# Kernel optimization log

Measured on AMD Instinct MI355X. Metric: run time of the kernel, lower is better.

Reference implementation:

```python
import jax, jax.numpy as jnp
import numpy as np

B, H, W = 8, 1024, 1024
RADIUS = 15.0
THRESHOLD_VOTES = 0.01
THRESHOLD_PEAKS = 0.2
KSIZE_VOTES = 15
KSIZE_PEAKS = 17


def setup_inputs() -> dict:
    key = jax.random.key(0)
    k1, k2 = jax.random.split(key)
    return {
        "stem_keypoint_output": jax.random.uniform(k1, (B, 1, H, W), dtype=jnp.float32),
        "stem_offset_output": jax.random.normal(k2, (B, 2, H, W), dtype=jnp.float32),
    }


def reference(stem_keypoint_output, stem_offset_output):
    b = stem_keypoint_output.shape[0]
    xs = jnp.arange(W, dtype=jnp.float32)[None, :]   # (1, W)
    ys = jnp.arange(H, dtype=jnp.float32)[:, None]   # (H, 1)

    # vote target coordinates, (B, H, W)
    votes_xs = jnp.round(xs + RADIUS * stem_offset_output[:, 0]).astype(jnp.int32)
    votes_ys = jnp.round(ys + RADIUS * stem_offset_output[:, 1]).astype(jnp.int32)
    weights = stem_keypoint_output[:, 0]

    # zero out-of-bounds and low-confidence votes (matches the index-assignment zeroing)
    valid = (votes_xs >= 0) & (votes_xs < W) & (votes_ys >= 0) & (votes_ys < H) & (weights >= THRESHOLD_VOTES)
    weights = jnp.where(valid, weights, 0.0)
    votes_xs = jnp.clip(votes_xs, 0, W - 1)
    votes_ys = jnp.clip(votes_ys, 0, H - 1)

    # scatter-accumulate votes (flat global index = b*H*W + y*W + x)
    flat_idx = (jnp.arange(b, dtype=jnp.int32)[:, None, None] * (H * W)
                + votes_ys * W + votes_xs).ravel()
    votes = jnp.zeros(b * H * W, jnp.float32).at[flat_idx].add(weights.ravel()).reshape(b, H, W)
    votes = votes / (np.pi * RADIUS * RADIUS)

    # box filter (conv with all-ones kernel, zero bias, SAME padding) == windowed sum
    votes = jax.lax.reduce_window(votes, 0.0, jax.lax.add,
                                  (1, KSIZE_VOTES, KSIZE_VOTES), (1, 1, 1), 'SAME')
    # max-pool dilation, SAME padding
    votes_dilated = jax.lax.reduce_window(votes, -jnp.inf, jax.lax.max,
                                          (1, KSIZE_PEAKS, KSIZE_PEAKS), (1, 1, 1), 'SAME')

    peaks = jnp.isclose(votes, votes_dilated) & (votes > THRESHOLD_PEAKS)
    # Return fixed-shape outputs: accumulated vote map (B,1,H,W) and peak mask (B,H,W).
    # (The original extracts (x, y, score) triplets per slice via nonzero(), which is
    #  data-dependent; the mask + vote map carry the identical information.)
    return votes[:, None], peaks
```

## Files before the change

### kernel.cpp

```cpp
#include <hip/hip_runtime.h>

constexpr int BB = 8;
constexpr int HH = 1024;
constexpr int WW = 1024;
constexpr int HW = HH * WW;
constexpr int TOTAL = BB * HW;

constexpr float RADIUS = 15.0f;
constexpr float THR_VOTES = 0.01f;
constexpr float THR_PEAKS = 0.2f;
constexpr float DIVISOR = 706.8583470577035f;

constexpr int TS = 64;
constexpr int AP = 48;
constexpr int RG = TS + 2 * AP;
constexpr int RGF = RG / 4;
constexpr int NF4 = RG * RGF;
constexpr int TPB = 256;
constexpr int NBLK = 2048;
constexpr int FCAP = 128;

constexpr int FIDX0 = NBLK;
constexpr int FW0   = NBLK + NBLK * FCAP;

__device__ __forceinline__ void process4(int px0, int py, float4 kw, float4 fox,
                                         float4 foy, int tx0, int ty0, int b,
                                         float* tile, int* lcnt,
                                         int* lidx, float* lw) {
    const float w[4]  = {kw.x, kw.y, kw.z, kw.w};
    const float ox[4] = {fox.x, fox.y, fox.z, fox.w};
    const float oy[4] = {foy.x, foy.y, foy.z, foy.w};
#pragma unroll
    for (int j = 0; j < 4; ++j) {
        const int px = px0 + j;
        const float fx = __fadd_rn((float)px, __fmul_rn(RADIUS, ox[j]));
        const float fy = __fadd_rn((float)py, __fmul_rn(RADIUS, oy[j]));
        const int vx = (int)rintf(fx);
        const int vy = (int)rintf(fy);
        if (vx < 0 || vx >= WW || vy < 0 || vy >= HH || w[j] < THR_VOTES) continue;
        const int dx = vx - px, dy = vy - py;
        if (dx >= -AP && dx <= AP && dy >= -AP && dy <= AP) {
            const int lx = vx - tx0, ly = vy - ty0;
            if (lx >= 0 && lx < TS && ly >= 0 && ly < TS)
                atomicAdd(&tile[ly * TS + lx], w[j]);
        } else if (px >= tx0 && px < tx0 + TS && py >= ty0 && py < ty0 + TS) {
            const int slot = atomicAdd(lcnt, 1);
            if (slot < FCAP) {
                lidx[slot] = b * HW + vy * WW + vx;
                lw[slot]   = w[j];
            }
        }
    }
}

__global__ __launch_bounds__(TPB, 8)
void gather_votes(const float* __restrict__ kp, const float* __restrict__ off,
                  float* __restrict__ vraw, float* __restrict__ farbuf) {
    __shared__ float tile[TS * TS];
    __shared__ int   lidx[FCAP];
    __shared__ float lw[FCAP];
    __shared__ int   lcnt;
    const int blk = blockIdx.x;
    const int b   = blk & 7;
    const int t   = blk >> 3;
    const int ty0 = (t >> 4) * TS;
    const int tx0 = (t & 15) * TS;

    if (threadIdx.x == 0) lcnt = 0;
    float4* tf4 = (float4*)tile;
    for (int j = threadIdx.x; j < TS * TS / 4; j += TPB)
        tf4[j] = make_float4(0.f, 0.f, 0.f, 0.f);
    __syncthreads();

    const float* kpb  = kp  + (long)b * HW;
    const float* offx = off + (long)b * 2 * HW;
    const float* offy = offx + HW;

    for (int u = threadIdx.x; u < NF4; u += 2 * TPB) {
        const int uB = u + TPB;
        const int rA  = u / RGF;
        const int cA  = u - rA * RGF;
        const int pyA = ty0 - AP + rA;
        const int pxA = tx0 - AP + 4 * cA;
        const bool okA = (pyA >= 0 && pyA < HH && pxA >= 0 && pxA <= WW - 4);
        const int rB  = uB / RGF;
        const int cB  = uB - rB * RGF;
        const int pyB = ty0 - AP + rB;
        const int pxB = tx0 - AP + 4 * cB;
        const bool okB = (uB < NF4 && pyB >= 0 && pyB < HH && pxB >= 0 && pxB <= WW - 4);

        float4 kA, xA, yA, kB, xB, yB;
        if (okA) {
            const long p = (long)pyA * WW + pxA;
            kA = *(const float4*)(kpb + p);
            xA = *(const float4*)(offx + p);
            yA = *(const float4*)(offy + p);
        }
        if (okB) {
            const long p = (long)pyB * WW + pxB;
            kB = *(const float4*)(kpb + p);
            xB = *(const float4*)(offx + p);
            yB = *(const float4*)(offy + p);
        }
        if (okA) process4(pxA, pyA, kA, xA, yA, tx0, ty0, b, tile, &lcnt, lidx, lw);
        if (okB) process4(pxB, pyB, kB, xB, yB, tx0, ty0, b, tile, &lcnt, lidx, lw);
    }
    __syncthreads();

    float* vb = vraw + (long)b * HW;
    for (int j = threadIdx.x; j < TS * TS / 4; j += TPB) {
        const int r  = j / (TS / 4);
        const int c4 = j % (TS / 4);
        *(float4*)&vb[(ty0 + r) * WW + tx0 + c4 * 4] = tf4[j];
    }
    const int n = min(lcnt, FCAP);
    int* fi = (int*)farbuf;
    if (threadIdx.x == 0) fi[blk] = n;
    for (int j = threadIdx.x; j < n; j += TPB) {
        fi[FIDX0 + blk * FCAP + j] = lidx[j];
        farbuf[FW0 + blk * FCAP + j] = lw[j];
    }
}

__global__ void far_scatter(const float* __restrict__ farbuf,
                            float* __restrict__ vraw) {
    const int s = blockIdx.x * blockDim.x + threadIdx.x;
    if (s >= NBLK * FCAP) return;
    const int blk = s / FCAP;
    const int j   = s % FCAP;
    const int* fi = (const int*)farbuf;
    if (j < min(fi[blk], FCAP))
        atomicAdd(&vraw[fi[FIDX0 + blk * FCAP + j]], farbuf[FW0 + blk * FCAP + j]);
}

__global__ __launch_bounds__(256)
void box_row(const float* __restrict__ in, float* __restrict__ out) {
    const long base = (long)blockIdx.x * WW;
    const int c0 = threadIdx.x * 4;
    float v[20];
#pragma unroll
    for (int k = 0; k < 5; ++k) {
        const int c = c0 - 8 + 4 * k;
        float4 f = (c >= 0 && c <= WW - 4) ? *(const float4*)&in[base + c]
                                           : make_float4(0.f, 0.f, 0.f, 0.f);
        v[4 * k + 0] = f.x; v[4 * k + 1] = f.y;
        v[4 * k + 2] = f.z; v[4 * k + 3] = f.w;
    }
    float s = 0.f;
#pragma unroll
    for (int k = 1; k <= 15; ++k) s += v[k];
    float4 o;
    o.x = s / DIVISOR;
    s += v[16] - v[1];  o.y = s / DIVISOR;
    s += v[17] - v[2];  o.z = s / DIVISOR;
    s += v[18] - v[3];  o.w = s / DIVISOR;
    *(float4*)&out[base + c0] = o;
}

__global__ __launch_bounds__(256)
void box_col(const float* __restrict__ in, float* __restrict__ out) {
    const int bi = blockIdx.x;
    const int xg = bi & 3;
    const int rg = (bi >> 2) & 127;
    const int b  = bi >> 9;
    const int x  = xg * 256 + threadIdx.x;
    const int r0 = rg * 8;
    const float* p = in + (long)b * HW + x;
    float v[22];
#pragma unroll
    for (int k = 0; k < 22; ++k) {
        const int r = r0 - 7 + k;
        v[k] = (r >= 0 && r < HH) ? p[(long)r * WW] : 0.f;
    }
    float s = 0.f;
#pragma unroll
    for (int k = 0; k < 15; ++k) s += v[k];
    float* q = out + (long)b * HW + x;
    q[(long)r0 * WW] = s;
#pragma unroll
    for (int j = 1; j < 8; ++j) {
        s += v[14 + j] - v[j - 1];
        q[(long)(r0 + j) * WW] = s;
    }
}

__global__ __launch_bounds__(256)
void max_row(const float* __restrict__ in, float* __restrict__ out) {
    const long base = (long)blockIdx.x * WW;
    const int c0 = threadIdx.x * 4;
    float v[20];
#pragma unroll
    for (int k = 0; k < 5; ++k) {
        const int c = c0 - 8 + 4 * k;
        float4 f = (c >= 0 && c <= WW - 4)
                       ? *(const float4*)&in[base + c]
                       : make_float4(-INFINITY, -INFINITY, -INFINITY, -INFINITY);
        v[4 * k + 0] = f.x; v[4 * k + 1] = f.y;
        v[4 * k + 2] = f.z; v[4 * k + 3] = f.w;
    }
    float m = v[3];
#pragma unroll
    for (int k = 4; k <= 16; ++k) m = fmaxf(m, v[k]);
    float4 o;
    o.x = fmaxf(fmaxf(m, v[0]),  fmaxf(v[1],  v[2]));
    o.y = fmaxf(fmaxf(m, v[1]),  fmaxf(v[2],  v[17]));
    o.z = fmaxf(fmaxf(m, v[2]),  fmaxf(v[17], v[18]));
    o.w = fmaxf(fmaxf(m, v[17]), fmaxf(v[18], v[19]));
    *(float4*)&out[base + c0] = o;
}

__global__ __launch_bounds__(256)
void max_col_peaks(const float* __restrict__ rowmaxed,
                   const float* __restrict__ votes,
                   float* __restrict__ peaks) {
    const int bi = blockIdx.x;
    const int xg = bi & 3;
    const int rg = (bi >> 2) & 127;
    const int b  = bi >> 9;
    const int x  = xg * 256 + threadIdx.x;
    const int r0 = rg * 8;
    const float* p = rowmaxed + (long)b * HW + x;
    float v[24];
#pragma unroll
    for (int k = 0; k < 24; ++k) {
        const int r = r0 - 8 + k;
        v[k] = (r >= 0 && r < HH) ? p[(long)r * WW] : -INFINITY;
    }
    float suf[17];
    suf[16] = v[16];
#pragma unroll
    for (int k = 15; k >= 0; --k) suf[k] = fmaxf(v[k], suf[k + 1]);

    const float* vp = votes + (long)b * HW + x;
    float* q = peaks + (long)b * HW + x;
    float pre = -INFINITY;
#pragma unroll
    for (int j = 0; j < 8; ++j) {
        if (j > 0) pre = fmaxf(pre, v[16 + j]);
        const float d = fmaxf(suf[j], pre);
        const float vv = vp[(long)(r0 + j) * WW];
        const bool close = fabsf(vv - d) <= (1e-8f + 1e-5f * fabsf(d));
        q[(long)(r0 + j) * WW] = (close && vv > THR_PEAKS) ? 1.0f : 0.0f;
    }
}

extern "C" void kernel_launch(void* const* d_in, const int* in_sizes, int n_in,
                              void* d_out, int out_size, void* d_ws, size_t ws_size,
                              hipStream_t stream) {
    const float* kp  = (const float*)d_in[0];
    const float* off = (const float*)d_in[1];
    float* V = (float*)d_out;
    float* P = (float*)d_out + TOTAL;
    float* W = (float*)d_ws;

    gather_votes <<<NBLK, TPB, 0, stream>>>(kp, off, W, P);
    far_scatter  <<<NBLK * FCAP / 256, 256, 0, stream>>>(P, W);
    box_row      <<<8192, 256, 0, stream>>>(W, P);
    box_col      <<<4096, 256, 0, stream>>>(P, V);
    max_row      <<<8192, 256, 0, stream>>>(V, W);
    max_col_peaks<<<4096, 256, 0, stream>>>(W, V, P);
}
```

Before: 233.0 us.

## Fuse separable box and max filters into 2D shared-memory tiled kernels

```diff
diff --git a/kernel.cpp b/kernel.cpp
--- a/kernel.cpp
+++ b/kernel.cpp
@@ -22,6 +22,10 @@
 
 constexpr int FIDX0 = NBLK;
 constexpr int FW0   = NBLK + NBLK * FCAP;
+
+constexpr int BT = 64;
+constexpr int BH = 8;
+constexpr int BR = BT + 2 * BH;
 
 __device__ __forceinline__ void process4(int px0, int py, float4 kw, float4 fox,
                                          float4 foy, int tx0, int ty0, int b,
@@ -134,113 +138,125 @@
 }
 
 __global__ __launch_bounds__(256)
-void box_row(const float* __restrict__ in, float* __restrict__ out) {
-    const long base = (long)blockIdx.x * WW;
-    const int c0 = threadIdx.x * 4;
-    float v[20];
-#pragma unroll
-    for (int k = 0; k < 5; ++k) {
-        const int c = c0 - 8 + 4 * k;
-        float4 f = (c >= 0 && c <= WW - 4) ? *(const float4*)&in[base + c]
-                                           : make_float4(0.f, 0.f, 0.f, 0.f);
-        v[4 * k + 0] = f.x; v[4 * k + 1] = f.y;
-        v[4 * k + 2] = f.z; v[4 * k + 3] = f.w;
-    }
-    float s = 0.f;
-#pragma unroll
-    for (int k = 1; k <= 15; ++k) s += v[k];
-    float4 o;
-    o.x = s / DIVISOR;
-    s += v[16] - v[1];  o.y = s / DIVISOR;
-    s += v[17] - v[2];  o.z = s / DIVISOR;
-    s += v[18] - v[3];  o.w = s / DIVISOR;
-    *(float4*)&out[base + c0] = o;
+void box2d(const float* __restrict__ in, float* __restrict__ out) {
+    __shared__ float reg[BR * BR];
+    __shared__ float rs[BR * BT];
+    const int blk = blockIdx.x;
+    const int b   = blk & 7;
+    const int t   = blk >> 3;
+    const int ty0 = (t >> 4) * BT;
+    const int tx0 = (t & 15) * BT;
+    const float* ib = in + (long)b * HW;
+
+    for (int o = threadIdx.x; o < BR * (BR / 4); o += 256) {
+        const int r  = o / (BR / 4);
+        const int c4 = o % (BR / 4);
+        const int gy = ty0 - BH + r;
+        const int gx = tx0 - BH + 4 * c4;
+        float4 f = make_float4(0.f, 0.f, 0.f, 0.f);
+        if (gy >= 0 && gy < HH && gx >= 0 && gx <= WW - 4)
+            f = *(const float4*)&ib[(long)gy * WW + gx];
+        *(float4*)&reg[r * BR + 4 * c4] = f;
+    }
+    __syncthreads();
+
+    for (int o = threadIdx.x; o < BR * (BT / 4); o += 256) {
+        const int r = o >> 4;
+        const int c = (o & 15) * 4;
+        float v[20];
+#pragma unroll
+        for (int k = 0; k < 5; ++k) {
+            float4 f = *(const float4*)&reg[r * BR + c + 4 * k];
+            v[4 * k] = f.x; v[4 * k + 1] = f.y; v[4 * k + 2] = f.z; v[4 * k + 3] = f.w;
+        }
+        float s = 0.f;
+#pragma unroll
+        for (int k = 1; k <= 15; ++k) s += v[k];
+        float4 q;
+        q.x = s / DIVISOR;
+        s += v[16] - v[1];  q.y = s / DIVISOR;
+        s += v[17] - v[2];  q.z = s / DIVISOR;
+        s += v[18] - v[3];  q.w = s / DIVISOR;
+        *(float4*)&rs[r * BT + c] = q;
+    }
+    __syncthreads();
+
+    float* ob = out + (long)b * HW;
+    for (int o = threadIdx.x; o < BT * (BT / 4); o += 256) {
+        const int r = o >> 4;
+        const int c = (o & 15) * 4;
+        float4 s = make_float4(0.f, 0.f, 0.f, 0.f);
+#pragma unroll
+        for (int k = 1; k <= 15; ++k) {
+            float4 f = *(const float4*)&rs[(r + k) * BT + c];
+            s.x += f.x; s.y += f.y; s.z += f.z; s.w += f.w;
+        }
+        *(float4*)&ob[(long)(ty0 + r) * WW + tx0 + c] = s;
+    }
 }
 
 __global__ __launch_bounds__(256)
-void box_col(const float* __restrict__ in, float* __restrict__ out) {
-    const int bi = blockIdx.x;
-    const int xg = bi & 3;
-    const int rg = (bi >> 2) & 127;
-    const int b  = bi >> 9;
-    const int x  = xg * 256 + threadIdx.x;
-    const int r0 = rg * 8;
-    const float* p = in + (long)b * HW + x;
-    float v[22];
-#pragma unroll
-    for (int k = 0; k < 22; ++k) {
-        const int r = r0 - 7 + k;
-        v[k] = (r >= 0 && r < HH) ? p[(long)r * WW] : 0.f;
-    }
-    float s = 0.f;
-#pragma unroll
-    for (int k = 0; k < 15; ++k) s += v[k];
-    float* q = out + (long)b * HW + x;
-    q[(long)r0 * WW] = s;
-#pragma unroll
-    for (int j = 1; j < 8; ++j) {
-        s += v[14 + j] - v[j - 1];
-        q[(long)(r0 + j) * WW] = s;
-    }
-}
-
-__global__ __launch_bounds__(256)
-void max_row(const float* __restrict__ in, float* __restrict__ out) {
-    const long base = (long)blockIdx.x * WW;
-    const int c0 = threadIdx.x * 4;
-    float v[20];
-#pragma unroll
-    for (int k = 0; k < 5; ++k) {
-        const int c = c0 - 8 + 4 * k;
-        float4 f = (c >= 0 && c <= WW - 4)
-                       ? *(const float4*)&in[base + c]
-                       : make_float4(-INFINITY, -INFINITY, -INFINITY, -INFINITY);
-        v[4 * k + 0] = f.x; v[4 * k + 1] = f.y;
-        v[4 * k + 2] = f.z; v[4 * k + 3] = f.w;
-    }
-    float m = v[3];
-#pragma unroll
-    for (int k = 4; k <= 16; ++k) m = fmaxf(m, v[k]);
-    float4 o;
-    o.x = fmaxf(fmaxf(m, v[0]),  fmaxf(v[1],  v[2]));
-    o.y = fmaxf(fmaxf(m, v[1]),  fmaxf(v[2],  v[17]));
-    o.z = fmaxf(fmaxf(m, v[2]),  fmaxf(v[17], v[18]));
-    o.w = fmaxf(fmaxf(m, v[17]), fmaxf(v[18], v[19]));
-    *(float4*)&out[base + c0] = o;
-}
-
-__global__ __launch_bounds__(256)
-void max_col_peaks(const float* __restrict__ rowmaxed,
-                   const float* __restrict__ votes,
-                   float* __restrict__ peaks) {
-    const int bi = blockIdx.x;
-    const int xg = bi & 3;
-    const int rg = (bi >> 2) & 127;
-    const int b  = bi >> 9;
-    const int x  = xg * 256 + threadIdx.x;
-    const int r0 = rg * 8;
-    const float* p = rowmaxed + (long)b * HW + x;
-    float v[24];
-#pragma unroll
-    for (int k = 0; k < 24; ++k) {
-        const int r = r0 - 8 + k;
-        v[k] = (r >= 0 && r < HH) ? p[(long)r * WW] : -INFINITY;
-    }
-    float suf[17];
-    suf[16] = v[16];
-#pragma unroll
-    for (int k = 15; k >= 0; --k) suf[k] = fmaxf(v[k], suf[k + 1]);
-
-    const float* vp = votes + (long)b * HW + x;
-    float* q = peaks + (long)b * HW + x;
-    float pre = -INFINITY;
-#pragma unroll
-    for (int j = 0; j < 8; ++j) {
-        if (j > 0) pre = fmaxf(pre, v[16 + j]);
-        const float d = fmaxf(suf[j], pre);
-        const float vv = vp[(long)(r0 + j) * WW];
-        const bool close = fabsf(vv - d) <= (1e-8f + 1e-5f * fabsf(d));
-        q[(long)(r0 + j) * WW] = (close && vv > THR_PEAKS) ? 1.0f : 0.0f;
+void max2d_peaks(const float* __restrict__ votes, float* __restrict__ peaks) {
+    __shared__ float reg[BR * BR];
+    __shared__ float rm[BR * BT];
+    const int blk = blockIdx.x;
+    const int b   = blk & 7;
+    const int t   = blk >> 3;
+    const int ty0 = (t >> 4) * BT;
+    const int tx0 = (t & 15) * BT;
+    const float* ib = votes + (long)b * HW;
+
+    for (int o = threadIdx.x; o < BR * (BR / 4); o += 256) {
+        const int r  = o / (BR / 4);
+        const int c4 = o % (BR / 4);
+        const int gy = ty0 - BH + r;
+        const int gx = tx0 - BH + 4 * c4;
+        float4 f = make_float4(-INFINITY, -INFINITY, -INFINITY, -INFINITY);
+        if (gy >= 0 && gy < HH && gx >= 0 && gx <= WW - 4)
+            f = *(const float4*)&ib[(long)gy * WW + gx];
+        *(float4*)&reg[r * BR + 4 * c4] = f;
+    }
+    __syncthreads();
+
+    for (int o = threadIdx.x; o < BR * (BT / 4); o += 256) {
+        const int r = o >> 4;
+        const int c = (o & 15) * 4;
+        float v[20];
+#pragma unroll
+        for (int k = 0; k < 5; ++k) {
+            float4 f = *(const float4*)&reg[r * BR + c + 4 * k];
+            v[4 * k] = f.x; v[4 * k + 1] = f.y; v[4 * k + 2] = f.z; v[4 * k + 3] = f.w;
+        }
+        float m = v[3];
+#pragma unroll
+        for (int k = 4; k <= 16; ++k) m = fmaxf(m, v[k]);
+        float4 q;
+        q.x = fmaxf(fmaxf(m, v[0]),  fmaxf(v[1],  v[2]));
+        q.y = fmaxf(fmaxf(m, v[1]),  fmaxf(v[2],  v[17]));
+        q.z = fmaxf(fmaxf(m, v[2]),  fmaxf(v[17], v[18]));
+        q.w = fmaxf(fmaxf(m, v[17]), fmaxf(v[18], v[19]));
+        *(float4*)&rm[r * BT + c] = q;
+    }
+    __syncthreads();
+
+    float* pb = peaks + (long)b * HW;
+    for (int o = threadIdx.x; o < BT * (BT / 4); o += 256) {
+        const int r = o >> 4;
+        const int c = (o & 15) * 4;
+        float4 d = *(const float4*)&rm[r * BT + c];
+#pragma unroll
+        for (int k = 1; k <= 16; ++k) {
+            float4 f = *(const float4*)&rm[(r + k) * BT + c];
+            d.x = fmaxf(d.x, f.x); d.y = fmaxf(d.y, f.y);
+            d.z = fmaxf(d.z, f.z); d.w = fmaxf(d.w, f.w);
+        }
+        const float4 vv = *(const float4*)&reg[(r + BH) * BR + c + BH];
+        float4 q;
+        q.x = (fabsf(vv.x - d.x) <= (1e-8f + 1e-5f * fabsf(d.x)) && vv.x > THR_PEAKS) ? 1.f : 0.f;
+        q.y = (fabsf(vv.y - d.y) <= (1e-8f + 1e-5f * fabsf(d.y)) && vv.y > THR_PEAKS) ? 1.f : 0.f;
+        q.z = (fabsf(vv.z - d.z) <= (1e-8f + 1e-5f * fabsf(d.z)) && vv.z > THR_PEAKS) ? 1.f : 0.f;
+        q.w = (fabsf(vv.w - d.w) <= (1e-8f + 1e-5f * fabsf(d.w)) && vv.w > THR_PEAKS) ? 1.f : 0.f;
+        *(float4*)&pb[(long)(ty0 + r) * WW + tx0 + c] = q;
     }
 }
 
@@ -253,10 +269,8 @@
     float* P = (float*)d_out + TOTAL;
     float* W = (float*)d_ws;
 
-    gather_votes <<<NBLK, TPB, 0, stream>>>(kp, off, W, P);
-    far_scatter  <<<NBLK * FCAP / 256, 256, 0, stream>>>(P, W);
-    box_row      <<<8192, 256, 0, stream>>>(W, P);
-    box_col      <<<4096, 256, 0, stream>>>(P, V);
-    max_row      <<<8192, 256, 0, stream>>>(V, W);
-    max_col_peaks<<<4096, 256, 0, stream>>>(W, V, P);
-}
+    gather_votes<<<NBLK, TPB, 0, stream>>>(kp, off, W, P);
+    far_scatter <<<NBLK * FCAP / 256, 256, 0, stream>>>(P, W);
+    box2d       <<<NBLK, 256, 0, stream>>>(W, V);
+    max2d_peaks <<<NBLK, 256, 0, stream>>>(V, P);
+}
```

New measurement: 222.2 us. -4.7%, faster.
